# Performance work log

Hardware: AMD Instinct MI355X
Metric: run time of the kernel (lower is better)

Reference implementation:

```python
import jax, jax.numpy as jnp
import numpy as np

DIM = 1024
HEADS = 16
HEAD_DIM = DIM // HEADS
SCALE = HEAD_DIM ** -0.5


def setup_inputs() -> dict:
    key = jax.random.key(0)
    k1, k2, k3, k4 = jax.random.split(key, 4)
    x = jax.random.normal(k1, (2, 2048, DIM), dtype=jnp.float32)
    # nn.Linear(dim, 3*dim, bias=False): weight shape (3*dim, dim), y = x @ W.T
    w_qkv = jax.random.normal(k2, (3 * DIM, DIM), dtype=jnp.float32) * (DIM ** -0.5)
    w_proj = jax.random.normal(k3, (DIM, DIM), dtype=jnp.float32) * (DIM ** -0.5)
    head_w = jnp.ones((HEADS,), dtype=jnp.float32)
    return {"x": x, "w_qkv": w_qkv, "w_proj": w_proj, "head_w": head_w}


def reference(x, w_qkv, w_proj, head_w) -> jnp.ndarray:
    B, N, C = x.shape
    qkv = jnp.einsum("bnc,dc->bnd", x, w_qkv)  # [B,N,3C]
    qkv = qkv.reshape(B, N, 3, HEADS, HEAD_DIM).transpose(2, 0, 3, 1, 4)
    q, k, v = qkv[0], qkv[1], qkv[2]  # each [B,H,N,Dh]
    attn = jnp.einsum("bhqd,bhkd->bhqk", q, k) * SCALE  # [B,H,N,N]
    attn = jax.nn.softmax(attn, axis=-1)
    out = jnp.einsum("bhqk,bhkd->bhqd", attn, v)  # [B,H,N,Dh]
    hw = jax.nn.softmax(head_w)[None, :, None, None]
    out = out * hw
    out = out.transpose(0, 2, 1, 3).reshape(B, N, C)
    return jnp.einsum("bnc,dc->bnd", out, w_proj)
```

## Files before the change

kernel.cpp:

```cpp
#include <hip/hip_runtime.h>

typedef _Float16 half_t;
typedef _Float16 half8 __attribute__((ext_vector_type(8)));
typedef _Float16 half4_t __attribute__((ext_vector_type(4)));
typedef _Float16 half2_t __attribute__((ext_vector_type(2)));
typedef float floatx4 __attribute__((ext_vector_type(4)));
typedef float floatx16 __attribute__((ext_vector_type(16)));
typedef unsigned int uint4v __attribute__((ext_vector_type(4)));
typedef unsigned int uint2v __attribute__((ext_vector_type(2)));

#define B_SZ 2
#define SEQ 2048
#define DIM_ 1024
#define NH 16
#define DH 64
#define ROWS (B_SZ * SEQ)
#define NJS 2

__device__ __forceinline__ void gl2lds16(const void* g, void* l) {
  __builtin_amdgcn_global_load_lds((const __attribute__((address_space(1))) unsigned int*)g,
                                   (__attribute__((address_space(3))) unsigned int*)l, 16, 0, 0);
}

__device__ __forceinline__ float fexp2(float x) {
#if __has_builtin(__builtin_amdgcn_exp2f)
  return __builtin_amdgcn_exp2f(x);
#else
  return __expf(x * 0.6931471805599453f);
#endif
}

__device__ __forceinline__ unsigned cvtpk_u32(float a, float b) {
#if __has_builtin(__builtin_amdgcn_cvt_pkrtz)
  return __builtin_bit_cast(unsigned, __builtin_amdgcn_cvt_pkrtz(a, b));
#else
  half2_t h; h.x = (half_t)a; h.y = (half_t)b;
  return __builtin_bit_cast(unsigned, h);
#endif
}

__global__ __launch_bounds__(256) void convert_all(const float4* __restrict__ x,
                                                   const float4* __restrict__ wq,
                                                   const float4* __restrict__ wp,
                                                   half4_t* __restrict__ dst,
                                                   int nx, int nq, int np) {
  int i = blockIdx.x * blockDim.x + threadIdx.x;
  float4 v;
  if (i < nx) v = x[i];
  else if (i < nx + nq) v = wq[i - nx];
  else if (i < nx + nq + np) v = wp[i - nx - nq];
  else return;
  half4_t h;
  h.x = (half_t)v.x; h.y = (half_t)v.y; h.z = (half_t)v.z; h.w = (half_t)v.w;
  dst[i] = h;
}

template <int MODE, int BN>
__global__ __launch_bounds__(256) void gemm32(const half_t* __restrict__ A,
                                              const half_t* __restrict__ Bt,
                                              half_t* __restrict__ q16,
                                              half_t* __restrict__ k16,
                                              half_t* __restrict__ vT16,
                                              float* __restrict__ outp) {
  constexpr int K = 1024;
  constexpr int NT = BN / 64;
  __shared__ __align__(16) half_t a_lds[128 * 64];
  __shared__ __align__(16) half_t b_lds[BN * 64];
  const int t = threadIdx.x;
  const int wave = t >> 6, lane = t & 63;
  const int l31 = lane & 31, hw = lane >> 5;
  const int wm = wave >> 1, wn = wave & 1;
  const int row0 = blockIdx.y * 128, col0 = blockIdx.x * BN;

  floatx16 acc[2][NT];
#pragma unroll
  for (int i = 0; i < 2; ++i)
#pragma unroll
    for (int j = 0; j < NT; ++j)
#pragma unroll
      for (int r = 0; r < 16; ++r) acc[i][j][r] = 0.f;

  for (int k0 = 0; k0 < K; k0 += 64) {
#pragma unroll
    for (int hi = 0; hi < 4; ++hi) {
      int s = t + hi * 256;
      int row = s >> 3, c = s & 7;
      int sc = c ^ (row & 7);
      gl2lds16(A + (size_t)(row0 + row) * K + (k0 + sc * 8), a_lds + (wave * 64 + hi * 256) * 8);
    }
#pragma unroll
    for (int hi = 0; hi < BN / 32; ++hi) {
      int s = t + hi * 256;
      int row = s >> 3, c = s & 7;
      int sc = c ^ (row & 7);
      gl2lds16(Bt + (size_t)(col0 + row) * K + (k0 + sc * 8), b_lds + (wave * 64 + hi * 256) * 8);
    }
    __syncthreads();
    half8 af[2][4], bf[NT][4];
#pragma unroll
    for (int mt = 0; mt < 2; ++mt) {
      int row = wm * 64 + mt * 32 + l31;
#pragma unroll
      for (int kf = 0; kf < 4; ++kf)
        af[mt][kf] = *(const half8*)(a_lds + row * 64 + ((kf * 2 + hw) ^ (row & 7)) * 8);
    }
#pragma unroll
    for (int nt = 0; nt < NT; ++nt) {
      int row = wn * (BN / 2) + nt * 32 + l31;
#pragma unroll
      for (int kf = 0; kf < 4; ++kf)
        bf[nt][kf] = *(const half8*)(b_lds + row * 64 + ((kf * 2 + hw) ^ (row & 7)) * 8);
    }
#pragma unroll
    for (int kf = 0; kf < 4; ++kf)
#pragma unroll
      for (int mt = 0; mt < 2; ++mt)
#pragma unroll
        for (int nt = 0; nt < NT; ++nt)
          acc[mt][nt] =
              __builtin_amdgcn_mfma_f32_32x32x16_f16(af[mt][kf], bf[nt][kf], acc[mt][nt], 0, 0, 0);
    __syncthreads();
  }

  if (MODE == 0) {
    const int which = col0 >> 10;
#pragma unroll
    for (int mt = 0; mt < 2; ++mt)
#pragma unroll
      for (int nt = 0; nt < NT; ++nt) {
        int growb = row0 + wm * 64 + mt * 32;
        int gcol = col0 + wn * (BN / 2) + nt * 32 + l31;
        int hc = gcol & 1023, h = hc >> 6, d = hc & 63;
        if (which == 2) {
#pragma unroll
          for (int rq = 0; rq < 4; ++rq) {
            int grow = growb + 8 * rq + 4 * hw;
            int b = grow >> 11, n0 = grow & 2047;
            int bh = b * NH + h;
            half4_t h4;
            h4.x = (half_t)acc[mt][nt][rq * 4 + 0];
            h4.y = (half_t)acc[mt][nt][rq * 4 + 1];
            h4.z = (half_t)acc[mt][nt][rq * 4 + 2];
            h4.w = (half_t)acc[mt][nt][rq * 4 + 3];
            *(half4_t*)(vT16 + ((size_t)bh * DH + d) * SEQ + n0) = h4;
          }
        } else {
#pragma unroll
          for (int r = 0; r < 16; ++r) {
            int grow = growb + (r & 3) + 8 * (r >> 2) + 4 * hw;
            int b = grow >> 11, n = grow & 2047;
            int bh = b * NH + h;
            float v = acc[mt][nt][r];
            if (which == 0)
              q16[((size_t)bh * SEQ + n) * DH + d] =
                  (half_t)(v * 0.1803368801111204f);
            else
              k16[((size_t)bh * SEQ + n) * DH + d] = (half_t)v;
          }
        }
      }
  } else {
#pragma unroll
    for (int mt = 0; mt < 2; ++mt)
#pragma unroll
      for (int nt = 0; nt < NT; ++nt) {
        int growb = row0 + wm * 64 + mt * 32;
        int gcol = col0 + wn * (BN / 2) + nt * 32 + l31;
#pragma unroll
        for (int r = 0; r < 16; ++r) {
          int grow = growb + (r & 3) + 8 * (r >> 2) + 4 * hw;
          outp[(size_t)grow * DIM_ + gcol] = acc[mt][nt][r];
        }
      }
  }
}

__global__ __launch_bounds__(256, 4) void attn_p1(const half_t* __restrict__ q16,
                                                  const half_t* __restrict__ k16,
                                                  const half_t* __restrict__ vT16,
                                                  half_t* __restrict__ opart,
                                                  float* __restrict__ psums) {
  __shared__ __align__(16) half_t k_lds[2][64 * 64];
  __shared__ __align__(16) half_t v_lds[2][64 * 64];

  const int t = threadIdx.x;
  const int wave = t >> 6, lane = t & 63;
  const int l31 = lane & 31, hw = lane >> 5;
  const int blk = blockIdx.x;
  const int js = blk & (NJS - 1), qt = (blk / NJS) & 15, bh = blk / (NJS * 16);
  const half_t* qp = q16 + (size_t)bh * SEQ * DH;
  const half_t* kp = k16 + (size_t)bh * SEQ * DH;
  const half_t* vp = vT16 + (size_t)bh * DH * SEQ;
  const int q0w = qt * 128 + wave * 32;
  const int jbase = js * (SEQ / NJS);
  constexpr int NJT = (SEQ / NJS) / 64;

  const int s0 = t, s1 = t + 256;
  const int r0_ = s0 >> 3, c0_ = (s0 & 7) ^ (r0_ & 7);
  const int r1_ = s1 >> 3, c1_ = (s1 & 7) ^ (r1_ & 7);

  half8 qf[4];
#pragma unroll
  for (int kf = 0; kf < 4; ++kf)
    qf[kf] = *(const half8*)(qp + (size_t)(q0w + l31) * DH + kf * 16 + hw * 8);

  floatx16 o[2];
#pragma unroll
  for (int i = 0; i < 2; ++i)
#pragma unroll
    for (int r = 0; r < 16; ++r) o[i][r] = 0.f;
  float psum = 0.f;

  gl2lds16(kp + (size_t)(jbase + r0_) * DH + c0_ * 8, &k_lds[0][(wave * 64) * 8]);
  gl2lds16(vp + (size_t)r0_ * SEQ + jbase + c0_ * 8, &v_lds[0][(wave * 64) * 8]);
  gl2lds16(kp + (size_t)(jbase + r1_) * DH + c1_ * 8, &k_lds[0][(wave * 64 + 256) * 8]);
  gl2lds16(vp + (size_t)r1_ * SEQ + jbase + c1_ * 8, &v_lds[0][(wave * 64 + 256) * 8]);

  int cur = 0;
  for (int jt = 0; jt < NJT; ++jt) {
    __syncthreads();

    if (jt + 1 < NJT) {
      const int j0 = jbase + (jt + 1) * 64, nb = cur ^ 1;
      gl2lds16(kp + (size_t)(j0 + r0_) * DH + c0_ * 8, &k_lds[nb][(wave * 64) * 8]);
      gl2lds16(vp + (size_t)r0_ * SEQ + j0 + c0_ * 8, &v_lds[nb][(wave * 64) * 8]);
      gl2lds16(kp + (size_t)(j0 + r1_) * DH + c1_ * 8, &k_lds[nb][(wave * 64 + 256) * 8]);
      gl2lds16(vp + (size_t)r1_ * SEQ + j0 + c1_ * 8, &v_lds[nb][(wave * 64 + 256) * 8]);
    }

    const half_t* kl = k_lds[cur];
    const half_t* vl = v_lds[cur];

    floatx16 st[2];
#pragma unroll
    for (int m = 0; m < 2; ++m)
#pragma unroll
      for (int r = 0; r < 16; ++r) st[m][r] = 0.f;
    __builtin_amdgcn_s_setprio(1);
#pragma unroll
    for (int kf = 0; kf < 4; ++kf)
#pragma unroll
      for (int m = 0; m < 2; ++m) {
        int row = m * 32 + l31;
        half8 kb = *(const half8*)(kl + row * 64 + ((kf * 2 + hw) ^ (row & 7)) * 8);
        st[m] = __builtin_amdgcn_mfma_f32_32x32x16_f16(kb, qf[kf], st[m], 0, 0, 0);
      }
    __builtin_amdgcn_s_setprio(0);

    half8 pa[4];
#pragma unroll
    for (int ks = 0; ks < 4; ++ks) {
      const int m = ks >> 1, rb = (ks & 1) * 8;
      float p0 = fexp2(st[m][rb + 0]);
      float p1 = fexp2(st[m][rb + 1]);
      float p2 = fexp2(st[m][rb + 2]);
      float p3 = fexp2(st[m][rb + 3]);
      float p4 = fexp2(st[m][rb + 4]);
      float p5 = fexp2(st[m][rb + 5]);
      float p6 = fexp2(st[m][rb + 6]);
      float p7 = fexp2(st[m][rb + 7]);
      psum += ((p0 + p1) + (p2 + p3)) + ((p4 + p5) + (p6 + p7));
      unsigned uA = cvtpk_u32(p0, p1);
      unsigned uB = cvtpk_u32(p2, p3);
      unsigned uC = cvtpk_u32(p4, p5);
      unsigned uD = cvtpk_u32(p6, p7);
#if __has_builtin(__builtin_amdgcn_permlane32_swap)
      uint2v sAC = __builtin_bit_cast(uint2v, __builtin_amdgcn_permlane32_swap(uA, uC, false, false));
      uint2v sBD = __builtin_bit_cast(uint2v, __builtin_amdgcn_permlane32_swap(uB, uD, false, false));
      uint4v u;
      u.x = sAC.x; u.y = sBD.x; u.z = sAC.y; u.w = sBD.y;
#else
      unsigned xA = (unsigned)__shfl_xor((int)uA, 32, 64);
      unsigned xB = (unsigned)__shfl_xor((int)uB, 32, 64);
      unsigned xC = (unsigned)__shfl_xor((int)uC, 32, 64);
      unsigned xD = (unsigned)__shfl_xor((int)uD, 32, 64);
      uint4v u;
      u.x = hw ? xC : uA;
      u.y = hw ? xD : uB;
      u.z = hw ? uC : xA;
      u.w = hw ? uD : xB;
#endif
      pa[ks] = __builtin_bit_cast(half8, u);
    }

    __builtin_amdgcn_s_setprio(1);
#pragma unroll
    for (int ks = 0; ks < 4; ++ks)
#pragma unroll
      for (int dt = 0; dt < 2; ++dt) {
        int row = dt * 32 + l31;
        half8 vb = *(const half8*)(vl + row * 64 + ((ks * 2 + hw) ^ (row & 7)) * 8);
        o[dt] = __builtin_amdgcn_mfma_f32_32x32x16_f16(pa[ks], vb, o[dt], 0, 0, 0);
      }
    __builtin_amdgcn_s_setprio(0);
    cur ^= 1;
  }

  psum += __shfl_xor(psum, 32, 64);
  if (hw == 0) psums[((size_t)(js * 32 + bh)) * SEQ + q0w + l31] = psum;

#pragma unroll
  for (int dt = 0; dt < 2; ++dt)
#pragma unroll
    for (int r = 0; r < 16; ++r) {
      int n = q0w + (r & 3) + 8 * (r >> 2) + 4 * hw;
      opart[((size_t)(js * 32 + bh) * SEQ + n) * DH + dt * 32 + l31] = (half_t)o[dt][r];
    }
}

__global__ __launch_bounds__(256) void combine(const half_t* __restrict__ opart,
                                               const float* __restrict__ psums,
                                               const float* __restrict__ head_w,
                                               half_t* __restrict__ attn16) {
  int idx = blockIdx.x * blockDim.x + threadIdx.x;
  int d4 = idx & 15, n = (idx >> 4) & 2047, bh = idx >> 15;
  int h = bh & 15, b = bh >> 4;
  const size_t jstr = (size_t)32 * SEQ * DH;
  size_t off = ((size_t)bh * SEQ + n) * DH + d4 * 4;

  float sx = 0.f, sy = 0.f, sz = 0.f, sw2 = 0.f, ps = 0.f;
#pragma unroll
  for (int js = 0; js < NJS; ++js) {
    half4_t ov = *(const half4_t*)(opart + js * jstr + off);
    sx += (float)ov.x; sy += (float)ov.y; sz += (float)ov.z; sw2 += (float)ov.w;
    ps += psums[(size_t)js * 32 * SEQ + (size_t)bh * SEQ + n];
  }

  float mw = head_w[0];
#pragma unroll
  for (int i = 1; i < NH; ++i) mw = fmaxf(mw, head_w[i]);
  float sw = 0.f;
#pragma unroll
  for (int i = 0; i < NH; ++i) sw += __expf(head_w[i] - mw);
  float hwv = __expf(head_w[h] - mw) / sw;

  float scl = hwv / ps;
  half4_t r;
  r.x = (half_t)(sx * scl);
  r.y = (half_t)(sy * scl);
  r.z = (half_t)(sz * scl);
  r.w = (half_t)(sw2 * scl);
  *(half4_t*)(attn16 + ((size_t)(b * SEQ + n)) * DIM_ + h * DH + d4 * 4) = r;
}

extern "C" void kernel_launch(void* const* d_in, const int* in_sizes, int n_in,
                              void* d_out, int out_size, void* d_ws, size_t ws_size,
                              hipStream_t stream) {
  const float* x = (const float*)d_in[0];
  const float* w_qkv = (const float*)d_in[1];
  const float* w_proj = (const float*)d_in[2];
  const float* head_w = (const float*)d_in[3];
  float* out = (float*)d_out;

  half_t* x16 = (half_t*)d_ws;
  half_t* wq16 = x16 + (size_t)ROWS * DIM_;
  half_t* wp16 = wq16 + (size_t)3 * DIM_ * DIM_;
  half_t* q16 = wp16 + (size_t)DIM_ * DIM_;
  half_t* k16 = q16 + (size_t)ROWS * DIM_;
  half_t* vT16 = k16 + (size_t)ROWS * DIM_;
  half_t* attn16 = vT16 + (size_t)ROWS * DIM_;
  half_t* opart = attn16 + (size_t)ROWS * DIM_;
  float* psums = (float*)(opart + (size_t)NJS * 32 * SEQ * DH);

  const int nx = ROWS * DIM_ / 4, nq = 3 * DIM_ * DIM_ / 4, np = DIM_ * DIM_ / 4;
  convert_all<<<(nx + nq + np) / 256, 256, 0, stream>>>((const float4*)x, (const float4*)w_qkv,
                                                        (const float4*)w_proj, (half4_t*)x16,
                                                        nx, nq, np);

  gemm32<0, 128><<<dim3(24, 32), 256, 0, stream>>>(x16, wq16, q16, k16, vT16, nullptr);
  attn_p1<<<32 * 16 * NJS, 256, 0, stream>>>(q16, k16, vT16, opart, psums);
  combine<<<(32 * SEQ * DH / 4) / 256, 256, 0, stream>>>(opart, psums, head_w, attn16);
  gemm32<1, 64><<<dim3(16, 32), 256, 0, stream>>>(attn16, wp16, nullptr, nullptr, nullptr, out);
}
```

Measured before the change: 181.4 us.

## Fuse split-KV combine into output projection GEMM A-tile load

```diff
diff --git a/kernel.cpp b/kernel.cpp
--- a/kernel.cpp
+++ b/kernel.cpp
@@ -36,6 +36,14 @@
 #else
   half2_t h; h.x = (half_t)a; h.y = (half_t)b;
   return __builtin_bit_cast(unsigned, h);
+#endif
+}
+
+__device__ __forceinline__ float frcp(float x) {
+#if __has_builtin(__builtin_amdgcn_rcpf)
+  return __builtin_amdgcn_rcpf(x);
+#else
+  return 1.f / x;
 #endif
 }
 
@@ -61,7 +69,10 @@
                                               half_t* __restrict__ q16,
                                               half_t* __restrict__ k16,
                                               half_t* __restrict__ vT16,
-                                              float* __restrict__ outp) {
+                                              float* __restrict__ outp,
+                                              const half_t* __restrict__ opart,
+                                              const float* __restrict__ psums,
+                                              const float* __restrict__ head_w) {
   constexpr int K = 1024;
   constexpr int NT = BN / 64;
   __shared__ __align__(16) half_t a_lds[128 * 64];
@@ -70,7 +81,23 @@
   const int wave = t >> 6, lane = t & 63;
   const int l31 = lane & 31, hw = lane >> 5;
   const int wm = wave >> 1, wn = wave & 1;
-  const int row0 = blockIdx.y * 128, col0 = blockIdx.x * BN;
+
+  const int lin = blockIdx.y * gridDim.x + blockIdx.x;
+  const int cpx = (gridDim.x * gridDim.y) >> 3;
+  const int nl = (lin & 7) * cpx + (lin >> 3);
+  const int bx = nl % gridDim.x, by = nl / gridDim.x;
+  const int row0 = by * 128, col0 = bx * BN;
+
+  float mw = 0.f, swd = 0.f;
+  if constexpr (MODE == 2) {
+    mw = head_w[0];
+#pragma unroll
+    for (int i = 1; i < NH; ++i) mw = fmaxf(mw, head_w[i]);
+#pragma unroll
+    for (int i = 0; i < NH; ++i) swd += __expf(head_w[i] - mw);
+  }
+  const size_t OJSTR = (size_t)32 * SEQ * DH;
+  const size_t PSJ = (size_t)32 * SEQ;
 
   floatx16 acc[2][NT];
 #pragma unroll
@@ -81,12 +108,33 @@
       for (int r = 0; r < 16; ++r) acc[i][j][r] = 0.f;
 
   for (int k0 = 0; k0 < K; k0 += 64) {
-#pragma unroll
-    for (int hi = 0; hi < 4; ++hi) {
-      int s = t + hi * 256;
-      int row = s >> 3, c = s & 7;
-      int sc = c ^ (row & 7);
-      gl2lds16(A + (size_t)(row0 + row) * K + (k0 + sc * 8), a_lds + (wave * 64 + hi * 256) * 8);
+    if constexpr (MODE != 2) {
+#pragma unroll
+      for (int hi = 0; hi < 4; ++hi) {
+        int s = t + hi * 256;
+        int row = s >> 3, c = s & 7;
+        int sc = c ^ (row & 7);
+        gl2lds16(A + (size_t)(row0 + row) * K + (k0 + sc * 8), a_lds + (wave * 64 + hi * 256) * 8);
+      }
+    } else {
+      const int h = k0 >> 6;
+      const float hs = __expf(head_w[h] - mw) * 4096.f / swd;
+#pragma unroll
+      for (int hi = 0; hi < 4; ++hi) {
+        int s = t + hi * 256;
+        int row = s >> 3, c = s & 7;
+        int sc = c ^ (row & 7);
+        int grow = row0 + row;
+        int b = grow >> 11, n = grow & 2047;
+        int bh = b * NH + h;
+        size_t obase = ((size_t)bh * SEQ + n) * DH + sc * 8;
+        half8 o0 = *(const half8*)(opart + obase);
+        half8 o1 = *(const half8*)(opart + OJSTR + obase);
+        float ps = psums[(size_t)bh * SEQ + n] + psums[PSJ + (size_t)bh * SEQ + n];
+        half_t sclh = (half_t)(hs * frcp(ps));
+        half8 r = (o0 + o1) * sclh;
+        *(half8*)(a_lds + (size_t)s * 8) = r;
+      }
     }
 #pragma unroll
     for (int hi = 0; hi < BN / 32; ++hi) {
@@ -160,6 +208,7 @@
         }
       }
   } else {
+    constexpr float OSCL = 1.f / 4096.f;
 #pragma unroll
     for (int mt = 0; mt < 2; ++mt)
 #pragma unroll
@@ -169,13 +218,13 @@
 #pragma unroll
         for (int r = 0; r < 16; ++r) {
           int grow = growb + (r & 3) + 8 * (r >> 2) + 4 * hw;
-          outp[(size_t)grow * DIM_ + gcol] = acc[mt][nt][r];
+          outp[(size_t)grow * DIM_ + gcol] = acc[mt][nt][r] * OSCL;
         }
       }
   }
 }
 
-__global__ __launch_bounds__(256, 4) void attn_p1(const half_t* __restrict__ q16,
+__global__ __launch_bounds__(256, 3) void attn_p1(const half_t* __restrict__ q16,
                                                   const half_t* __restrict__ k16,
                                                   const half_t* __restrict__ vT16,
                                                   half_t* __restrict__ opart,
@@ -308,41 +357,6 @@
     }
 }
 
-__global__ __launch_bounds__(256) void combine(const half_t* __restrict__ opart,
-                                               const float* __restrict__ psums,
-                                               const float* __restrict__ head_w,
-                                               half_t* __restrict__ attn16) {
-  int idx = blockIdx.x * blockDim.x + threadIdx.x;
-  int d4 = idx & 15, n = (idx >> 4) & 2047, bh = idx >> 15;
-  int h = bh & 15, b = bh >> 4;
-  const size_t jstr = (size_t)32 * SEQ * DH;
-  size_t off = ((size_t)bh * SEQ + n) * DH + d4 * 4;
-
-  float sx = 0.f, sy = 0.f, sz = 0.f, sw2 = 0.f, ps = 0.f;
-#pragma unroll
-  for (int js = 0; js < NJS; ++js) {
-    half4_t ov = *(const half4_t*)(opart + js * jstr + off);
-    sx += (float)ov.x; sy += (float)ov.y; sz += (float)ov.z; sw2 += (float)ov.w;
-    ps += psums[(size_t)js * 32 * SEQ + (size_t)bh * SEQ + n];
-  }
-
-  float mw = head_w[0];
-#pragma unroll
-  for (int i = 1; i < NH; ++i) mw = fmaxf(mw, head_w[i]);
-  float sw = 0.f;
-#pragma unroll
-  for (int i = 0; i < NH; ++i) sw += __expf(head_w[i] - mw);
-  float hwv = __expf(head_w[h] - mw) / sw;
-
-  float scl = hwv / ps;
-  half4_t r;
-  r.x = (half_t)(sx * scl);
-  r.y = (half_t)(sy * scl);
-  r.z = (half_t)(sz * scl);
-  r.w = (half_t)(sw2 * scl);
-  *(half4_t*)(attn16 + ((size_t)(b * SEQ + n)) * DIM_ + h * DH + d4 * 4) = r;
-}
-
 extern "C" void kernel_launch(void* const* d_in, const int* in_sizes, int n_in,
                               void* d_out, int out_size, void* d_ws, size_t ws_size,
                               hipStream_t stream) {
@@ -358,8 +372,7 @@
   half_t* q16 = wp16 + (size_t)DIM_ * DIM_;
   half_t* k16 = q16 + (size_t)ROWS * DIM_;
   half_t* vT16 = k16 + (size_t)ROWS * DIM_;
-  half_t* attn16 = vT16 + (size_t)ROWS * DIM_;
-  half_t* opart = attn16 + (size_t)ROWS * DIM_;
+  half_t* opart = vT16 + (size_t)ROWS * DIM_;
   float* psums = (float*)(opart + (size_t)NJS * 32 * SEQ * DH);
 
   const int nx = ROWS * DIM_ / 4, nq = 3 * DIM_ * DIM_ / 4, np = DIM_ * DIM_ / 4;
@@ -367,8 +380,9 @@
                                                         (const float4*)w_proj, (half4_t*)x16,
                                                         nx, nq, np);
 
-  gemm32<0, 128><<<dim3(24, 32), 256, 0, stream>>>(x16, wq16, q16, k16, vT16, nullptr);
+  gemm32<0, 128><<<dim3(24, 32), 256, 0, stream>>>(x16, wq16, q16, k16, vT16, nullptr,
+                                                   nullptr, nullptr, nullptr);
   attn_p1<<<32 * 16 * NJS, 256, 0, stream>>>(q16, k16, vT16, opart, psums);
-  combine<<<(32 * SEQ * DH / 4) / 256, 256, 0, stream>>>(opart, psums, head_w, attn16);
-  gemm32<1, 64><<<dim3(16, 32), 256, 0, stream>>>(attn16, wp16, nullptr, nullptr, nullptr, out);
-}
+  gemm32<2, 64><<<dim3(16, 32), 256, 0, stream>>>(nullptr, wp16, nullptr, nullptr, nullptr, out,
+                                                  opart, psums, head_w);
+}
```

Result: slower. 189.9 us (+4.7%).

## Double query rows per wave in attention and swizzle GEMM block order

Applied to the files above, without the earlier changes.

```diff
diff --git a/kernel.cpp b/kernel.cpp
--- a/kernel.cpp
+++ b/kernel.cpp
@@ -70,7 +70,12 @@
   const int wave = t >> 6, lane = t & 63;
   const int l31 = lane & 31, hw = lane >> 5;
   const int wm = wave >> 1, wn = wave & 1;
-  const int row0 = blockIdx.y * 128, col0 = blockIdx.x * BN;
+
+  const int lin = blockIdx.y * gridDim.x + blockIdx.x;
+  const int cpx = (gridDim.x * gridDim.y) >> 3;
+  const int nl = (lin & 7) * cpx + (lin >> 3);
+  const int bx = nl % gridDim.x, by = nl / gridDim.x;
+  const int row0 = by * 128, col0 = bx * BN;
 
   floatx16 acc[2][NT];
 #pragma unroll
@@ -175,7 +180,7 @@
   }
 }
 
-__global__ __launch_bounds__(256, 4) void attn_p1(const half_t* __restrict__ q16,
+__global__ __launch_bounds__(256, 2) void attn_p1(const half_t* __restrict__ q16,
                                                   const half_t* __restrict__ k16,
                                                   const half_t* __restrict__ vT16,
                                                   half_t* __restrict__ opart,
@@ -187,11 +192,11 @@
   const int wave = t >> 6, lane = t & 63;
   const int l31 = lane & 31, hw = lane >> 5;
   const int blk = blockIdx.x;
-  const int js = blk & (NJS - 1), qt = (blk / NJS) & 15, bh = blk / (NJS * 16);
+  const int js = blk & (NJS - 1), qt = (blk / NJS) & 7, bh = blk / (NJS * 8);
   const half_t* qp = q16 + (size_t)bh * SEQ * DH;
   const half_t* kp = k16 + (size_t)bh * SEQ * DH;
   const half_t* vp = vT16 + (size_t)bh * DH * SEQ;
-  const int q0w = qt * 128 + wave * 32;
+  const int q0w = qt * 256 + wave * 64;
   const int jbase = js * (SEQ / NJS);
   constexpr int NJT = (SEQ / NJS) / 64;
 
@@ -199,17 +204,22 @@
   const int r0_ = s0 >> 3, c0_ = (s0 & 7) ^ (r0_ & 7);
   const int r1_ = s1 >> 3, c1_ = (s1 & 7) ^ (r1_ & 7);
 
-  half8 qf[4];
-#pragma unroll
-  for (int kf = 0; kf < 4; ++kf)
-    qf[kf] = *(const half8*)(qp + (size_t)(q0w + l31) * DH + kf * 16 + hw * 8);
-
-  floatx16 o[2];
-#pragma unroll
-  for (int i = 0; i < 2; ++i)
-#pragma unroll
-    for (int r = 0; r < 16; ++r) o[i][r] = 0.f;
-  float psum = 0.f;
+  half8 qf[2][4];
+#pragma unroll
+  for (int qi = 0; qi < 2; ++qi)
+#pragma unroll
+    for (int kf = 0; kf < 4; ++kf)
+      qf[qi][kf] =
+          *(const half8*)(qp + (size_t)(q0w + qi * 32 + l31) * DH + kf * 16 + hw * 8);
+
+  floatx16 o[2][2];
+#pragma unroll
+  for (int qi = 0; qi < 2; ++qi)
+#pragma unroll
+    for (int i = 0; i < 2; ++i)
+#pragma unroll
+      for (int r = 0; r < 16; ++r) o[qi][i][r] = 0.f;
+  float psum[2] = {0.f, 0.f};
 
   gl2lds16(kp + (size_t)(jbase + r0_) * DH + c0_ * 8, &k_lds[0][(wave * 64) * 8]);
   gl2lds16(vp + (size_t)r0_ * SEQ + jbase + c0_ * 8, &v_lds[0][(wave * 64) * 8]);
@@ -231,56 +241,62 @@
     const half_t* kl = k_lds[cur];
     const half_t* vl = v_lds[cur];
 
-    floatx16 st[2];
-#pragma unroll
-    for (int m = 0; m < 2; ++m)
-#pragma unroll
-      for (int r = 0; r < 16; ++r) st[m][r] = 0.f;
-    __builtin_amdgcn_s_setprio(1);
-#pragma unroll
-    for (int kf = 0; kf < 4; ++kf)
-#pragma unroll
-      for (int m = 0; m < 2; ++m) {
+    half8 pa[2][4];
+#pragma unroll
+    for (int m = 0; m < 2; ++m) {
+      floatx16 st[2];
+#pragma unroll
+      for (int qi = 0; qi < 2; ++qi)
+#pragma unroll
+        for (int r = 0; r < 16; ++r) st[qi][r] = 0.f;
+      __builtin_amdgcn_s_setprio(1);
+#pragma unroll
+      for (int kf = 0; kf < 4; ++kf) {
         int row = m * 32 + l31;
         half8 kb = *(const half8*)(kl + row * 64 + ((kf * 2 + hw) ^ (row & 7)) * 8);
-        st[m] = __builtin_amdgcn_mfma_f32_32x32x16_f16(kb, qf[kf], st[m], 0, 0, 0);
-      }
-    __builtin_amdgcn_s_setprio(0);
-
-    half8 pa[4];
-#pragma unroll
-    for (int ks = 0; ks < 4; ++ks) {
-      const int m = ks >> 1, rb = (ks & 1) * 8;
-      float p0 = fexp2(st[m][rb + 0]);
-      float p1 = fexp2(st[m][rb + 1]);
-      float p2 = fexp2(st[m][rb + 2]);
-      float p3 = fexp2(st[m][rb + 3]);
-      float p4 = fexp2(st[m][rb + 4]);
-      float p5 = fexp2(st[m][rb + 5]);
-      float p6 = fexp2(st[m][rb + 6]);
-      float p7 = fexp2(st[m][rb + 7]);
-      psum += ((p0 + p1) + (p2 + p3)) + ((p4 + p5) + (p6 + p7));
-      unsigned uA = cvtpk_u32(p0, p1);
-      unsigned uB = cvtpk_u32(p2, p3);
-      unsigned uC = cvtpk_u32(p4, p5);
-      unsigned uD = cvtpk_u32(p6, p7);
+#pragma unroll
+        for (int qi = 0; qi < 2; ++qi)
+          st[qi] = __builtin_amdgcn_mfma_f32_32x32x16_f16(kb, qf[qi][kf], st[qi], 0, 0, 0);
+      }
+      __builtin_amdgcn_s_setprio(0);
+#pragma unroll
+      for (int qi = 0; qi < 2; ++qi)
+#pragma unroll
+        for (int hh = 0; hh < 2; ++hh) {
+          const int rb = hh * 8;
+          float p0 = fexp2(st[qi][rb + 0]);
+          float p1 = fexp2(st[qi][rb + 1]);
+          float p2 = fexp2(st[qi][rb + 2]);
+          float p3 = fexp2(st[qi][rb + 3]);
+          float p4 = fexp2(st[qi][rb + 4]);
+          float p5 = fexp2(st[qi][rb + 5]);
+          float p6 = fexp2(st[qi][rb + 6]);
+          float p7 = fexp2(st[qi][rb + 7]);
+          psum[qi] += ((p0 + p1) + (p2 + p3)) + ((p4 + p5) + (p6 + p7));
+          unsigned uA = cvtpk_u32(p0, p1);
+          unsigned uB = cvtpk_u32(p2, p3);
+          unsigned uC = cvtpk_u32(p4, p5);
+          unsigned uD = cvtpk_u32(p6, p7);
 #if __has_builtin(__builtin_amdgcn_permlane32_swap)
-      uint2v sAC = __builtin_bit_cast(uint2v, __builtin_amdgcn_permlane32_swap(uA, uC, false, false));
-      uint2v sBD = __builtin_bit_cast(uint2v, __builtin_amdgcn_permlane32_swap(uB, uD, false, false));
-      uint4v u;
-      u.x = sAC.x; u.y = sBD.x; u.z = sAC.y; u.w = sBD.y;
+          uint2v sAC =
+              __builtin_bit_cast(uint2v, __builtin_amdgcn_permlane32_swap(uA, uC, false, false));
+          uint2v sBD =
+              __builtin_bit_cast(uint2v, __builtin_amdgcn_permlane32_swap(uB, uD, false, false));
+          uint4v u;
+          u.x = sAC.x; u.y = sBD.x; u.z = sAC.y; u.w = sBD.y;
 #else
-      unsigned xA = (unsigned)__shfl_xor((int)uA, 32, 64);
-      unsigned xB = (unsigned)__shfl_xor((int)uB, 32, 64);
-      unsigned xC = (unsigned)__shfl_xor((int)uC, 32, 64);
-      unsigned xD = (unsigned)__shfl_xor((int)uD, 32, 64);
-      uint4v u;
-      u.x = hw ? xC : uA;
-      u.y = hw ? xD : uB;
-      u.z = hw ? uC : xA;
-      u.w = hw ? uD : xB;
+          unsigned xA = (unsigned)__shfl_xor((int)uA, 32, 64);
+          unsigned xB = (unsigned)__shfl_xor((int)uB, 32, 64);
+          unsigned xC = (unsigned)__shfl_xor((int)uC, 32, 64);
+          unsigned xD = (unsigned)__shfl_xor((int)uD, 32, 64);
+          uint4v u;
+          u.x = hw ? xC : uA;
+          u.y = hw ? xD : uB;
+          u.z = hw ? uC : xA;
+          u.w = hw ? uD : xB;
 #endif
-      pa[ks] = __builtin_bit_cast(half8, u);
+          pa[qi][m * 2 + hh] = __builtin_bit_cast(half8, u);
+        }
     }
 
     __builtin_amdgcn_s_setprio(1);
@@ -290,22 +306,29 @@
       for (int dt = 0; dt < 2; ++dt) {
         int row = dt * 32 + l31;
         half8 vb = *(const half8*)(vl + row * 64 + ((ks * 2 + hw) ^ (row & 7)) * 8);
-        o[dt] = __builtin_amdgcn_mfma_f32_32x32x16_f16(pa[ks], vb, o[dt], 0, 0, 0);
+#pragma unroll
+        for (int qi = 0; qi < 2; ++qi)
+          o[qi][dt] = __builtin_amdgcn_mfma_f32_32x32x16_f16(pa[qi][ks], vb, o[qi][dt], 0, 0, 0);
       }
     __builtin_amdgcn_s_setprio(0);
     cur ^= 1;
   }
 
-  psum += __shfl_xor(psum, 32, 64);
-  if (hw == 0) psums[((size_t)(js * 32 + bh)) * SEQ + q0w + l31] = psum;
-
-#pragma unroll
-  for (int dt = 0; dt < 2; ++dt)
-#pragma unroll
-    for (int r = 0; r < 16; ++r) {
-      int n = q0w + (r & 3) + 8 * (r >> 2) + 4 * hw;
-      opart[((size_t)(js * 32 + bh) * SEQ + n) * DH + dt * 32 + l31] = (half_t)o[dt][r];
-    }
+#pragma unroll
+  for (int qi = 0; qi < 2; ++qi) {
+    psum[qi] += __shfl_xor(psum[qi], 32, 64);
+    if (hw == 0) psums[((size_t)(js * 32 + bh)) * SEQ + q0w + qi * 32 + l31] = psum[qi];
+  }
+
+#pragma unroll
+  for (int qi = 0; qi < 2; ++qi)
+#pragma unroll
+    for (int dt = 0; dt < 2; ++dt)
+#pragma unroll
+      for (int r = 0; r < 16; ++r) {
+        int n = q0w + qi * 32 + (r & 3) + 8 * (r >> 2) + 4 * hw;
+        opart[((size_t)(js * 32 + bh) * SEQ + n) * DH + dt * 32 + l31] = (half_t)o[qi][dt][r];
+      }
 }
 
 __global__ __launch_bounds__(256) void combine(const half_t* __restrict__ opart,
@@ -368,7 +391,7 @@
                                                         nx, nq, np);
 
   gemm32<0, 128><<<dim3(24, 32), 256, 0, stream>>>(x16, wq16, q16, k16, vT16, nullptr);
-  attn_p1<<<32 * 16 * NJS, 256, 0, stream>>>(q16, k16, vT16, opart, psums);
+  attn_p1<<<32 * 8 * NJS, 256, 0, stream>>>(q16, k16, vT16, opart, psums);
   combine<<<(32 * SEQ * DH / 4) / 256, 256, 0, stream>>>(opart, psums, head_w, attn16);
   gemm32<1, 64><<<dim3(16, 32), 256, 0, stream>>>(attn16, wp16, nullptr, nullptr, nullptr, out);
 }
```

After: 183.2 us. No clear change (+1.0%).
